# Performance work log

Measured on AMD Instinct MI355X. Metric: run time of the kernel, lower is better.

## Reference

```python
import jax, jax.numpy as jnp
import numpy as np

N = 100000      # nodes
E = 1000000     # edges per branch
C_IN = 128      # in_channels
C_OUT = 64      # out_channels
BN_EPS = 1e-5


def setup_inputs() -> dict:
    key = jax.random.key(0)
    ks = jax.random.split(key, 8)
    inp = {"x": jax.random.normal(ks[0], (N, C_IN), jnp.float32)}
    for i, name in enumerate(["edge_index_p", "edge_index_s", "edge_index_v"]):
        inp[name] = jax.random.randint(ks[1 + i], (2, E), 0, N, dtype=jnp.int32)
    # input BatchNorm1d affine params
    inp["in_gamma"] = jnp.ones((C_IN,), jnp.float32)
    inp["in_beta"] = jnp.zeros((C_IN,), jnp.float32)
    # per-branch GIN MLP params, stacked over the 3 branches (p, s, v)
    inp["W1"] = jax.random.normal(ks[4], (3, C_IN, C_OUT), jnp.float32) * 0.05
    inp["b1"] = jnp.zeros((3, C_OUT), jnp.float32)
    inp["W2"] = jax.random.normal(ks[5], (3, C_OUT, C_OUT), jnp.float32) * 0.05
    inp["b2"] = jnp.zeros((3, C_OUT), jnp.float32)
    # per-branch output BatchNorm1d affine params
    inp["bn_gamma"] = jnp.ones((3, C_OUT), jnp.float32)
    inp["bn_beta"] = jnp.zeros((3, C_OUT), jnp.float32)
    return inp


def _batchnorm(h, gamma, beta):
    # training-mode BatchNorm1d: batch stats over the node dim, biased variance
    mu = h.mean(axis=0)
    var = ((h - mu) ** 2).mean(axis=0)
    return gamma * (h - mu) * jax.lax.rsqrt(var + BN_EPS) + beta


def reference(x, edge_index_p, edge_index_s, edge_index_v,
              in_gamma, in_beta, W1, b1, W2, b2, bn_gamma, bn_beta):
    n = x.shape[0]
    xn = _batchnorm(x, in_gamma, in_beta)  # in_norm
    outs = []
    for i, ei in enumerate([edge_index_p, edge_index_s, edge_index_v]):
        src, dst = ei[0], ei[1]
        # GINConv (eps=0): sum-aggregate neighbor features, add self
        agg = jax.ops.segment_sum(xn[src], dst, num_segments=n)  # [N, C_IN]
        h = xn + agg
        # MLP([C_IN, C_OUT, C_OUT]) with ReLU between, plain last layer
        h = jax.nn.relu(h @ W1[i] + b1[i])
        h = h @ W2[i] + b2[i]
        # post-GIN BatchNorm1d + Tanh
        outs.append(jnp.tanh(_batchnorm(h, bn_gamma[i], bn_beta[i])))
    return tuple(outs)  # (x_p, x_s, x_v)
```

## Files before the change

### kernel.cpp

```cpp
#include <hip/hip_runtime.h>
#include <math.h>

#define NN   100000
#define NE   1000000
#define CIN  128
#define COUT 64
#define BN_EPS 1e-5f
#define NB    391
#define NBLK1 128
#define CHUNK_E ((NE + NBLK1 - 1) / NBLK1)
#define NT    32
#define NTILE (NN / NT)

#define Y1B_OFF    0
#define COL_OFF    9600000
#define ROWPTR_OFF 12600000
#define OFF_OFF    12900016
#define W1P_OFF    13050160
#define C1_OFF     (W1P_OFF + 3*CIN*COUT)
#define INSUM_OFF  (C1_OFF + 3*COUT)
#define INSQ_OFF   (INSUM_OFF + CIN)
#define OSUM_OFF   (INSQ_OFF + CIN)
#define OSQ_OFF    (OSUM_OFF + 3*COUT)
#define SCALE_OFF  (OSQ_OFF + 3*COUT)
#define SHIFT_OFF  (SCALE_OFF + CIN)
#define OBNS_OFF   (SHIFT_OFF + CIN)
#define OBNB_OFF   (OBNS_OFF + 3*COUT)
#define ZERO_OFF   INSUM_OFF
#define ZERO_CNT   (2*CIN + 6*COUT)

__device__ __forceinline__ unsigned bf16_rne(float f) {
    unsigned u = __float_as_uint(f);
    return (u + 0x7FFFu + ((u >> 16) & 1u)) >> 16;
}
__device__ __forceinline__ float lo16f(unsigned u) { return __uint_as_float(u << 16); }
__device__ __forceinline__ float hi16f(unsigned u) { return __uint_as_float(u & 0xFFFF0000u); }

__global__ __launch_bounds__(256) void k_in_stats(const float* __restrict__ x,
                                                  float* __restrict__ ws) {
    int tid = blockIdx.x * blockDim.x + threadIdx.x;
    int c = tid & (CIN - 1);
    int r0 = tid >> 7;
    int rstride = (gridDim.x * blockDim.x) >> 7;
    float s = 0.f, ss = 0.f;
    for (int r = r0; r < NN; r += rstride) {
        float v = x[(size_t)r * CIN + c];
        s += v; ss += v * v;
    }
    unsafeAtomicAdd(&ws[INSUM_OFF + c], s);
    unsafeAtomicAdd(&ws[INSQ_OFF + c], ss);
}

__global__ void k_in_finalize(const float* __restrict__ g, const float* __restrict__ b,
                              float* __restrict__ ws) {
    int c = threadIdx.x;
    float mu  = ws[INSUM_OFF + c] * (1.f / NN);
    float var = ws[INSQ_OFF + c] * (1.f / NN) - mu * mu;
    float sc  = g[c] * rsqrtf(var + BN_EPS);
    ws[SCALE_OFF + c] = sc;
    ws[SHIFT_OFF + c] = b[c] - mu * sc;
}

__global__ void k_fold(const float* __restrict__ W1, float* __restrict__ ws) {
    int idx = blockIdx.x * blockDim.x + threadIdx.x;
    int k = (idx >> 6) & (CIN - 1);
    ws[W1P_OFF + idx] = ws[SCALE_OFF + k] * W1[idx];
}

__global__ void k_c1(const float* __restrict__ W1, float* __restrict__ ws) {
    int i = blockIdx.x, o = threadIdx.x;
    float acc = 0.f;
    for (int k = 0; k < CIN; ++k)
        acc = fmaf(ws[SHIFT_OFF + k], W1[i * CIN * COUT + k * COUT + o], acc);
    ws[C1_OFF + i * COUT + o] = acc;
}

__global__ __launch_bounds__(256) void k_sort_hist(const int* __restrict__ e0,
                                                   const int* __restrict__ e1,
                                                   const int* __restrict__ e2,
                                                   int* __restrict__ wsi) {
    int z = blockIdx.y;
    const int* ei = (z == 0) ? e0 : (z == 1) ? e1 : e2;
    __shared__ int h[NB];
    for (int i = threadIdx.x; i < NB; i += 256) h[i] = 0;
    __syncthreads();
    int beg = blockIdx.x * CHUNK_E;
    int end = min(NE, beg + CHUNK_E);
    for (int e = beg + threadIdx.x; e < end; e += 256)
        atomicAdd(&h[ei[NE + e] >> 8], 1);
    __syncthreads();
    int* off = wsi + OFF_OFF + z * (NB * NBLK1);
    for (int i = threadIdx.x; i < NB; i += 256)
        off[i * NBLK1 + blockIdx.x] = h[i];
}

__global__ __launch_bounds__(1024) void k_sort_scan(int* __restrict__ wsi) {
    int z = blockIdx.x;
    int* off = wsi + OFF_OFF + z * (NB * NBLK1);
    const int TOT = NB * NBLK1;
    const int CH = (TOT + 1023) / 1024;
    __shared__ int sh[1024];
    int t = threadIdx.x;
    int base = t * CH;
    int s = 0;
    for (int i = 0; i < CH; ++i) {
        int idx = base + i;
        if (idx < TOT) s += off[idx];
    }
    sh[t] = s;
    __syncthreads();
    for (int o = 1; o < 1024; o <<= 1) {
        int v = (t >= o) ? sh[t - o] : 0;
        __syncthreads();
        sh[t] += v;
        __syncthreads();
    }
    int run = sh[t] - s;
    for (int i = 0; i < CH; ++i) {
        int idx = base + i;
        if (idx < TOT) {
            int v = off[idx];
            off[idx] = run;
            run += v;
        }
    }
}

__global__ __launch_bounds__(256) void k_sort_scatter(const int* __restrict__ e0,
                                                      const int* __restrict__ e1,
                                                      const int* __restrict__ e2,
                                                      int* __restrict__ wsi) {
    int z = blockIdx.y;
    const int* ei = (z == 0) ? e0 : (z == 1) ? e1 : e2;
    const int* off = wsi + OFF_OFF + z * (NB * NBLK1);
    unsigned* temp = (unsigned*)wsi + (size_t)z * NE;
    __shared__ int cur[NB];
    for (int i = threadIdx.x; i < NB; i += 256)
        cur[i] = off[i * NBLK1 + blockIdx.x];
    __syncthreads();
    int beg = blockIdx.x * CHUNK_E;
    int end = min(NE, beg + CHUNK_E);
    for (int e = beg + threadIdx.x; e < end; e += 256) {
        int d = ei[NE + e];
        int s = ei[e];
        int pos = atomicAdd(&cur[d >> 8], 1);
        temp[pos] = ((unsigned)(d & 255) << 24) | (unsigned)s;
    }
}

__global__ __launch_bounds__(256) void k_bucket(int* __restrict__ wsi) {
    int z = blockIdx.y, bk = blockIdx.x;
    const int* off = wsi + OFF_OFF + z * (NB * NBLK1);
    const unsigned* temp = (const unsigned*)wsi + (size_t)z * NE;
    int* col    = wsi + COL_OFF + z * NE;
    int* rowptr = wsi + ROWPTR_OFF + z * (NN + 1);
    int bs = off[bk * NBLK1];
    int be = (bk + 1 < NB) ? off[(bk + 1) * NBLK1] : NE;
    __shared__ int h[256], sc[256], cur[256];
    int t = threadIdx.x;
    h[t] = 0;
    __syncthreads();
    for (int e = bs + t; e < be; e += 256)
        atomicAdd(&h[temp[e] >> 24], 1);
    __syncthreads();
    int v = h[t];
    sc[t] = v;
    __syncthreads();
    for (int o = 1; o < 256; o <<= 1) {
        int u = (t >= o) ? sc[t - o] : 0;
        __syncthreads();
        sc[t] += u;
        __syncthreads();
    }
    int excl = sc[t] - v;
    int gd = bk * 256 + t;
    if (gd <= NN) rowptr[gd] = bs + excl;
    cur[t] = excl;
    __syncthreads();
    for (int e = bs + t; e < be; e += 256) {
        unsigned p = temp[e];
        int pos = atomicAdd(&cur[p >> 24], 1);
        col[bs + pos] = (int)(p & 0x00FFFFFFu);
    }
}

__global__ __launch_bounds__(256, 2) void k_gemm1(const float* __restrict__ x,
                                                  const float* __restrict__ W1p_all,
                                                  const float* __restrict__ c1_all,
                                                  unsigned* __restrict__ y1b_all) {
    int lane = threadIdx.x & 63;
    int wave = (blockIdx.x * blockDim.x + threadIdx.x) >> 6;
    int nw   = (gridDim.x * blockDim.x) >> 6;
    float c1v0 = c1_all[lane];
    float c1v1 = c1_all[COUT + lane];
    float c1v2 = c1_all[2 * COUT + lane];
    const int NGRP = NN / 8;
    for (int g = wave; g < NGRP; g += nw) {
        int n0 = __builtin_amdgcn_readfirstlane(g) * 8;
        const float* __restrict__ xr = x + (size_t)n0 * CIN;
        float a0[8], a1[8], a2[8];
        #pragma unroll
        for (int i = 0; i < 8; ++i) { a0[i] = c1v0; a1[i] = c1v1; a2[i] = c1v2; }
        #pragma unroll 1
        for (int kc = 0; kc < CIN; kc += 16) {
            float w0[16], w1[16], w2[16];
            #pragma unroll
            for (int j = 0; j < 16; ++j) {
                w0[j] = W1p_all[(kc + j) * COUT + lane];
                w1[j] = W1p_all[CIN * COUT + (kc + j) * COUT + lane];
                w2[j] = W1p_all[2 * CIN * COUT + (kc + j) * COUT + lane];
            }
            #pragma unroll
            for (int i = 0; i < 8; ++i) {
                #pragma unroll
                for (int j = 0; j < 16; ++j) {
                    float xv = xr[i * CIN + kc + j];
                    a0[i] = fmaf(xv, w0[j], a0[i]);
                    a1[i] = fmaf(xv, w1[j], a1[i]);
                    a2[i] = fmaf(xv, w2[j], a2[i]);
                }
            }
        }
        #define STORE_NODE(zz, az, i) { \
            float vhi_ = __shfl(az[i], (lane & 31) + 32); \
            if (lane < 32) { \
                unsigned wrd_ = bf16_rne(az[i]) | (bf16_rne(vhi_) << 16); \
                y1b_all[((size_t)(zz) * NN + n0 + (i)) * 32 + lane] = wrd_; \
            } }
        #pragma unroll
        for (int i = 0; i < 8; ++i) {
            STORE_NODE(0, a0, i)
            STORE_NODE(1, a1, i)
            STORE_NODE(2, a2, i)
        }
        #undef STORE_NODE
    }
}

__global__ __launch_bounds__(256) void k_gather(const float* __restrict__ b1all,
                                                float* __restrict__ tall,
                                                float* __restrict__ ws) {
    int z = blockIdx.y;
    const unsigned* __restrict__ y1b = (const unsigned*)ws + Y1B_OFF + (size_t)z * NN * 32;
    float* __restrict__ t = tall + (size_t)z * NN * COUT;
    const int* __restrict__ rowptr = (const int*)ws + ROWPTR_OFF + z * (NN + 1);
    const int* __restrict__ col    = (const int*)ws + COL_OFF + z * NE;
    int lane = threadIdx.x & 63;
    int w32  = lane & 31;
    int half = lane >> 5;
    float b1lo = b1all[z * COUT + w32];
    float b1hi = b1all[z * COUT + 32 + w32];
    int wave = (blockIdx.x * blockDim.x + threadIdx.x) >> 6;
    int nw   = (gridDim.x * blockDim.x) >> 6;
    const int NP = NN / 2;
    for (int p = wave; p < NP; p += nw) {
        int n = p * 2 + half;
        int beg = rowptr[n], end = rowptr[n + 1];
        unsigned su = y1b[(size_t)n * 32 + w32];
        float alo = lo16f(su), ahi = hi16f(su);
        float blo = 0.f, bhi = 0.f, clo = 0.f, chi = 0.f, dlo = 0.f, dhi = 0.f;
        int j = beg;
        for (; j + 3 < end; j += 4) {
            int c0 = col[j], c1 = col[j + 1], c2 = col[j + 2], c3 = col[j + 3];
            unsigned u0 = y1b[(size_t)c0 * 32 + w32];
            unsigned u1 = y1b[(size_t)c1 * 32 + w32];
            unsigned u2 = y1b[(size_t)c2 * 32 + w32];
            unsigned u3 = y1b[(size_t)c3 * 32 + w32];
            alo += lo16f(u0); ahi += hi16f(u0);
            blo += lo16f(u1); bhi += hi16f(u1);
            clo += lo16f(u2); chi += hi16f(u2);
            dlo += lo16f(u3); dhi += hi16f(u3);
        }
        for (; j < end; ++j) {
            unsigned u = y1b[(size_t)col[j] * 32 + w32];
            alo += lo16f(u); ahi += hi16f(u);
        }
        t[(size_t)n * 64 + w32]      = fmaxf((alo + blo) + (clo + dlo) + b1lo, 0.f);
        t[(size_t)n * 64 + 32 + w32] = fmaxf((ahi + bhi) + (chi + dhi) + b1hi, 0.f);
    }
}

__global__ __launch_bounds__(256) void k_mlp2(const float* __restrict__ W2all,
                                              const float* __restrict__ b2all,
                                              float* __restrict__ outall,
                                              float* __restrict__ ws) {
    int z = blockIdx.y;
    __shared__ float w2s[COUT * COUT];
    __shared__ float ts[NT][COUT];
    const float* __restrict__ W2 = W2all + z * COUT * COUT;
    float* __restrict__ out = outall + (size_t)z * NN * COUT;
    int tid = threadIdx.x;
    for (int i = tid; i < COUT * COUT; i += 256) w2s[i] = W2[i];
    int lane = tid & 63;
    int wave = tid >> 6;
    int n0 = wave * 8;
    float b2v = b2all[z * COUT + lane];
    float ls = 0.f, lss = 0.f;
    float4 r0, r1;
    {
        const float4* __restrict__ src =
            (const float4*)(out + (size_t)blockIdx.x * NT * COUT);
        r0 = src[tid];
        r1 = src[tid + 256];
    }
    for (int tile = blockIdx.x; tile < NTILE; tile += gridDim.x) {
        __syncthreads();
        {
            float4* dst = (float4*)ts;
            dst[tid] = r0;
            dst[tid + 256] = r1;
        }
        __syncthreads();
        int nxt = tile + gridDim.x;
        if (nxt < NTILE) {
            const float4* __restrict__ src =
                (const float4*)(out + (size_t)nxt * NT * COUT);
            r0 = src[tid];
            r1 = src[tid + 256];
        }
        float a0 = b2v, a1 = b2v, a2 = b2v, a3 = b2v;
        float a4 = b2v, a5 = b2v, a6 = b2v, a7 = b2v;
        #pragma unroll
        for (int jq = 0; jq < 16; ++jq) {
            float wj0 = w2s[(4 * jq)     * COUT + lane];
            float wj1 = w2s[(4 * jq + 1) * COUT + lane];
            float wj2 = w2s[(4 * jq + 2) * COUT + lane];
            float wj3 = w2s[(4 * jq + 3) * COUT + lane];
            float4 t0 = *(const float4*)&ts[n0 + 0][4 * jq];
            float4 t1 = *(const float4*)&ts[n0 + 1][4 * jq];
            float4 t2 = *(const float4*)&ts[n0 + 2][4 * jq];
            float4 t3 = *(const float4*)&ts[n0 + 3][4 * jq];
            float4 t4 = *(const float4*)&ts[n0 + 4][4 * jq];
            float4 t5 = *(const float4*)&ts[n0 + 5][4 * jq];
            float4 t6 = *(const float4*)&ts[n0 + 6][4 * jq];
            float4 t7 = *(const float4*)&ts[n0 + 7][4 * jq];
            a0 = fmaf(t0.x, wj0, a0); a0 = fmaf(t0.y, wj1, a0);
            a0 = fmaf(t0.z, wj2, a0); a0 = fmaf(t0.w, wj3, a0);
            a1 = fmaf(t1.x, wj0, a1); a1 = fmaf(t1.y, wj1, a1);
            a1 = fmaf(t1.z, wj2, a1); a1 = fmaf(t1.w, wj3, a1);
            a2 = fmaf(t2.x, wj0, a2); a2 = fmaf(t2.y, wj1, a2);
            a2 = fmaf(t2.z, wj2, a2); a2 = fmaf(t2.w, wj3, a2);
            a3 = fmaf(t3.x, wj0, a3); a3 = fmaf(t3.y, wj1, a3);
            a3 = fmaf(t3.z, wj2, a3); a3 = fmaf(t3.w, wj3, a3);
            a4 = fmaf(t4.x, wj0, a4); a4 = fmaf(t4.y, wj1, a4);
            a4 = fmaf(t4.z, wj2, a4); a4 = fmaf(t4.w, wj3, a4);
            a5 = fmaf(t5.x, wj0, a5); a5 = fmaf(t5.y, wj1, a5);
            a5 = fmaf(t5.z, wj2, a5); a5 = fmaf(t5.w, wj3, a5);
            a6 = fmaf(t6.x, wj0, a6); a6 = fmaf(t6.y, wj1, a6);
            a6 = fmaf(t6.z, wj2, a6); a6 = fmaf(t6.w, wj3, a6);
            a7 = fmaf(t7.x, wj0, a7); a7 = fmaf(t7.y, wj1, a7);
            a7 = fmaf(t7.z, wj2, a7); a7 = fmaf(t7.w, wj3, a7);
        }
        size_t base = (size_t)tile * NT * COUT + (size_t)n0 * COUT;
        out[base + lane] = a0;
        out[base + COUT + lane] = a1;
        out[base + 2 * COUT + lane] = a2;
        out[base + 3 * COUT + lane] = a3;
        out[base + 4 * COUT + lane] = a4;
        out[base + 5 * COUT + lane] = a5;
        out[base + 6 * COUT + lane] = a6;
        out[base + 7 * COUT + lane] = a7;
        ls += ((a0 + a1) + (a2 + a3)) + ((a4 + a5) + (a6 + a7));
        lss += ((a0 * a0 + a1 * a1) + (a2 * a2 + a3 * a3))
             + ((a4 * a4 + a5 * a5) + (a6 * a6 + a7 * a7));
    }
    unsafeAtomicAdd(&ws[OSUM_OFF + z * COUT + lane], ls);
    unsafeAtomicAdd(&ws[OSQ_OFF + z * COUT + lane], lss);
}

__global__ void k_obn_final(const float* __restrict__ g, const float* __restrict__ b,
                            float* __restrict__ ws) {
    int br = blockIdx.x;
    int o = threadIdx.x;
    float mu  = ws[OSUM_OFF + br * COUT + o] * (1.f / NN);
    float var = ws[OSQ_OFF  + br * COUT + o] * (1.f / NN) - mu * mu;
    float sc  = g[br * COUT + o] * rsqrtf(var + BN_EPS);
    ws[OBNS_OFF + br * COUT + o] = sc;
    ws[OBNB_OFF + br * COUT + o] = b[br * COUT + o] - mu * sc;
}

__global__ __launch_bounds__(256) void k_apply(float* __restrict__ outall,
                                               const float* __restrict__ ws) {
    int z = blockIdx.y;
    float* out = outall + (size_t)z * NN * COUT;
    const float* __restrict__ sc = ws + OBNS_OFF + z * COUT;
    const float* __restrict__ sh = ws + OBNB_OFF + z * COUT;
    int idx = blockIdx.x * blockDim.x + threadIdx.x;
    int stride = gridDim.x * blockDim.x;
    const int total = NN * COUT / 4;
    float4* o4 = (float4*)out;
    for (int v = idx; v < total; v += stride) {
        int c = (v & 15) * 4;
        float4 f = o4[v];
        f.x = tanhf(fmaf(f.x, sc[c],     sh[c]));
        f.y = tanhf(fmaf(f.y, sc[c + 1], sh[c + 1]));
        f.z = tanhf(fmaf(f.z, sc[c + 2], sh[c + 2]));
        f.w = tanhf(fmaf(f.w, sc[c + 3], sh[c + 3]));
        o4[v] = f;
    }
}

extern "C" void kernel_launch(void* const* d_in, const int* in_sizes, int n_in,
                              void* d_out, int out_size, void* d_ws, size_t ws_size,
                              hipStream_t stream) {
    const float* x   = (const float*)d_in[0];
    const int*   eip = (const int*)d_in[1];
    const int*   eis = (const int*)d_in[2];
    const int*   eiv = (const int*)d_in[3];
    const float* ig  = (const float*)d_in[4];
    const float* ib  = (const float*)d_in[5];
    const float* W1  = (const float*)d_in[6];
    const float* b1  = (const float*)d_in[7];
    const float* W2  = (const float*)d_in[8];
    const float* b2  = (const float*)d_in[9];
    const float* bng = (const float*)d_in[10];
    const float* bnb = (const float*)d_in[11];
    float* out = (float*)d_out;
    float* ws  = (float*)d_ws;
    int*   wsi = (int*)d_ws;

    hipMemsetAsync(ws + ZERO_OFF, 0, ZERO_CNT * sizeof(float), stream);

    k_in_stats<<<256, 256, 0, stream>>>(x, ws);
    k_in_finalize<<<1, 128, 0, stream>>>(ig, ib, ws);
    k_fold<<<96, 256, 0, stream>>>(W1, ws);
    k_c1<<<3, 64, 0, stream>>>(W1, ws);

    k_sort_hist<<<dim3(NBLK1, 3), 256, 0, stream>>>(eip, eis, eiv, wsi);
    k_sort_scan<<<3, 1024, 0, stream>>>(wsi);
    k_sort_scatter<<<dim3(NBLK1, 3), 256, 0, stream>>>(eip, eis, eiv, wsi);
    k_bucket<<<dim3(NB, 3), 256, 0, stream>>>(wsi);

    k_gemm1<<<1024, 256, 0, stream>>>(x, ws + W1P_OFF, ws + C1_OFF,
                                      (unsigned*)ws + Y1B_OFF);
    k_gather<<<dim3(2048, 3), 256, 0, stream>>>(b1, out, ws);
    k_mlp2<<<dim3(512, 3), 256, 0, stream>>>(W2, b2, out, ws);
    k_obn_final<<<3, 64, 0, stream>>>(bng, bnb, ws);
    k_apply<<<dim3(1024, 3), 256, 0, stream>>>(out, ws);
}
```

Before: 548.4 us.

## Rewrite second GEMM as per-lane row matvec and split out BN stats

The second MLP layer now assigns one node row per lane. Each lane loads its 64-element row into registers and computes outputs in four groups of 16, reading W2 through scalar/uniform loads instead of LDS. This removes the shared-memory staging and barriers. The output BatchNorm sum and sum-of-squares reduction moves into a separate kernel that rereads the full output, which adds an extra pass over 3x100000x64 floats plus a launch. Per-lane strided row loads are uncoalesced and register pressure is high.

```diff
diff --git a/kernel.cpp b/kernel.cpp
--- a/kernel.cpp
+++ b/kernel.cpp
@@ -9,8 +9,6 @@
 #define NB    391
 #define NBLK1 128
 #define CHUNK_E ((NE + NBLK1 - 1) / NBLK1)
-#define NT    32
-#define NTILE (NN / NT)
 
 #define Y1B_OFF    0
 #define COL_OFF    9600000
@@ -282,90 +280,68 @@
 
 __global__ __launch_bounds__(256) void k_mlp2(const float* __restrict__ W2all,
                                               const float* __restrict__ b2all,
-                                              float* __restrict__ outall,
-                                              float* __restrict__ ws) {
-    int z = blockIdx.y;
-    __shared__ float w2s[COUT * COUT];
-    __shared__ float ts[NT][COUT];
+                                              float* __restrict__ outall) {
+    int z = blockIdx.y;
     const float* __restrict__ W2 = W2all + z * COUT * COUT;
+    const float* __restrict__ b2 = b2all + z * COUT;
     float* __restrict__ out = outall + (size_t)z * NN * COUT;
-    int tid = threadIdx.x;
-    for (int i = tid; i < COUT * COUT; i += 256) w2s[i] = W2[i];
-    int lane = tid & 63;
-    int wave = tid >> 6;
-    int n0 = wave * 8;
-    float b2v = b2all[z * COUT + lane];
-    float ls = 0.f, lss = 0.f;
-    float4 r0, r1;
-    {
-        const float4* __restrict__ src =
-            (const float4*)(out + (size_t)blockIdx.x * NT * COUT);
-        r0 = src[tid];
-        r1 = src[tid + 256];
-    }
-    for (int tile = blockIdx.x; tile < NTILE; tile += gridDim.x) {
-        __syncthreads();
-        {
-            float4* dst = (float4*)ts;
-            dst[tid] = r0;
-            dst[tid + 256] = r1;
-        }
-        __syncthreads();
-        int nxt = tile + gridDim.x;
-        if (nxt < NTILE) {
-            const float4* __restrict__ src =
-                (const float4*)(out + (size_t)nxt * NT * COUT);
-            r0 = src[tid];
-            r1 = src[tid + 256];
-        }
-        float a0 = b2v, a1 = b2v, a2 = b2v, a3 = b2v;
-        float a4 = b2v, a5 = b2v, a6 = b2v, a7 = b2v;
-        #pragma unroll
-        for (int jq = 0; jq < 16; ++jq) {
-            float wj0 = w2s[(4 * jq)     * COUT + lane];
-            float wj1 = w2s[(4 * jq + 1) * COUT + lane];
-            float wj2 = w2s[(4 * jq + 2) * COUT + lane];
-            float wj3 = w2s[(4 * jq + 3) * COUT + lane];
-            float4 t0 = *(const float4*)&ts[n0 + 0][4 * jq];
-            float4 t1 = *(const float4*)&ts[n0 + 1][4 * jq];
-            float4 t2 = *(const float4*)&ts[n0 + 2][4 * jq];
-            float4 t3 = *(const float4*)&ts[n0 + 3][4 * jq];
-            float4 t4 = *(const float4*)&ts[n0 + 4][4 * jq];
-            float4 t5 = *(const float4*)&ts[n0 + 5][4 * jq];
-            float4 t6 = *(const float4*)&ts[n0 + 6][4 * jq];
-            float4 t7 = *(const float4*)&ts[n0 + 7][4 * jq];
-            a0 = fmaf(t0.x, wj0, a0); a0 = fmaf(t0.y, wj1, a0);
-            a0 = fmaf(t0.z, wj2, a0); a0 = fmaf(t0.w, wj3, a0);
-            a1 = fmaf(t1.x, wj0, a1); a1 = fmaf(t1.y, wj1, a1);
-            a1 = fmaf(t1.z, wj2, a1); a1 = fmaf(t1.w, wj3, a1);
-            a2 = fmaf(t2.x, wj0, a2); a2 = fmaf(t2.y, wj1, a2);
-            a2 = fmaf(t2.z, wj2, a2); a2 = fmaf(t2.w, wj3, a2);
-            a3 = fmaf(t3.x, wj0, a3); a3 = fmaf(t3.y, wj1, a3);
-            a3 = fmaf(t3.z, wj2, a3); a3 = fmaf(t3.w, wj3, a3);
-            a4 = fmaf(t4.x, wj0, a4); a4 = fmaf(t4.y, wj1, a4);
-            a4 = fmaf(t4.z, wj2, a4); a4 = fmaf(t4.w, wj3, a4);
-            a5 = fmaf(t5.x, wj0, a5); a5 = fmaf(t5.y, wj1, a5);
-            a5 = fmaf(t5.z, wj2, a5); a5 = fmaf(t5.w, wj3, a5);
-            a6 = fmaf(t6.x, wj0, a6); a6 = fmaf(t6.y, wj1, a6);
-            a6 = fmaf(t6.z, wj2, a6); a6 = fmaf(t6.w, wj3, a6);
-            a7 = fmaf(t7.x, wj0, a7); a7 = fmaf(t7.y, wj1, a7);
-            a7 = fmaf(t7.z, wj2, a7); a7 = fmaf(t7.w, wj3, a7);
-        }
-        size_t base = (size_t)tile * NT * COUT + (size_t)n0 * COUT;
-        out[base + lane] = a0;
-        out[base + COUT + lane] = a1;
-        out[base + 2 * COUT + lane] = a2;
-        out[base + 3 * COUT + lane] = a3;
-        out[base + 4 * COUT + lane] = a4;
-        out[base + 5 * COUT + lane] = a5;
-        out[base + 6 * COUT + lane] = a6;
-        out[base + 7 * COUT + lane] = a7;
-        ls += ((a0 + a1) + (a2 + a3)) + ((a4 + a5) + (a6 + a7));
-        lss += ((a0 * a0 + a1 * a1) + (a2 * a2 + a3 * a3))
-             + ((a4 * a4 + a5 * a5) + (a6 * a6 + a7 * a7));
-    }
-    unsafeAtomicAdd(&ws[OSUM_OFF + z * COUT + lane], ls);
-    unsafeAtomicAdd(&ws[OSQ_OFF + z * COUT + lane], lss);
+    int lane = threadIdx.x & 63;
+    int wave = (blockIdx.x * blockDim.x + threadIdx.x) >> 6;
+    int nw   = (gridDim.x * blockDim.x) >> 6;
+    const int NTL = (NN + 63) / 64;
+    for (int tl = wave; tl < NTL; tl += nw) {
+        int n = tl * 64 + lane;
+        int nc = (n < NN) ? n : NN - 1;
+        bool valid = (n < NN);
+        const float4* __restrict__ tr = (const float4*)(out + (size_t)nc * COUT);
+        float4 T0 = tr[0],  T1 = tr[1],  T2 = tr[2],  T3 = tr[3];
+        float4 T4 = tr[4],  T5 = tr[5],  T6 = tr[6],  T7 = tr[7];
+        float4 T8 = tr[8],  T9 = tr[9],  T10 = tr[10], T11 = tr[11];
+        float4 T12 = tr[12], T13 = tr[13], T14 = tr[14], T15 = tr[15];
+        float4* __restrict__ ow = (float4*)(out + (size_t)nc * COUT);
+        #pragma unroll 1
+        for (int p = 0; p < 4; ++p) {
+            const float* __restrict__ w2p = W2 + p * 16;
+            float acc[16];
+            #pragma unroll
+            for (int o = 0; o < 16; ++o) acc[o] = b2[p * 16 + o];
+#define FMA16(tj, jj) { float tjv_ = (tj); \
+            _Pragma("unroll") \
+            for (int o = 0; o < 16; ++o) \
+                acc[o] = fmaf(tjv_, w2p[(jj) * COUT + o], acc[o]); }
+#define DO4(Tv, jb) FMA16(Tv.x, 4*(jb)) FMA16(Tv.y, 4*(jb)+1) \
+                    FMA16(Tv.z, 4*(jb)+2) FMA16(Tv.w, 4*(jb)+3)
+            DO4(T0, 0)  DO4(T1, 1)  DO4(T2, 2)  DO4(T3, 3)
+            DO4(T4, 4)  DO4(T5, 5)  DO4(T6, 6)  DO4(T7, 7)
+            DO4(T8, 8)  DO4(T9, 9)  DO4(T10, 10) DO4(T11, 11)
+            DO4(T12, 12) DO4(T13, 13) DO4(T14, 14) DO4(T15, 15)
+#undef DO4
+#undef FMA16
+            if (valid) {
+                ow[p * 4 + 0] = make_float4(acc[0], acc[1], acc[2], acc[3]);
+                ow[p * 4 + 1] = make_float4(acc[4], acc[5], acc[6], acc[7]);
+                ow[p * 4 + 2] = make_float4(acc[8], acc[9], acc[10], acc[11]);
+                ow[p * 4 + 3] = make_float4(acc[12], acc[13], acc[14], acc[15]);
+            }
+        }
+    }
+}
+
+__global__ __launch_bounds__(256) void k_h2_stats(const float* __restrict__ outall,
+                                                  float* __restrict__ ws) {
+    int z = blockIdx.y;
+    const float* __restrict__ h = outall + (size_t)z * NN * COUT;
+    int tid = blockIdx.x * blockDim.x + threadIdx.x;
+    int o = tid & 63;
+    int r0 = tid >> 6;
+    int rs = (gridDim.x * blockDim.x) >> 6;
+    float s = 0.f, ss = 0.f;
+    for (int r = r0; r < NN; r += rs) {
+        float v = h[(size_t)r * COUT + o];
+        s += v; ss += v * v;
+    }
+    unsafeAtomicAdd(&ws[OSUM_OFF + z * COUT + o], s);
+    unsafeAtomicAdd(&ws[OSQ_OFF + z * COUT + o], ss);
 }
 
 __global__ void k_obn_final(const float* __restrict__ g, const float* __restrict__ b,
@@ -434,7 +410,8 @@
     k_gemm1<<<1024, 256, 0, stream>>>(x, ws + W1P_OFF, ws + C1_OFF,
                                       (unsigned*)ws + Y1B_OFF);
     k_gather<<<dim3(2048, 3), 256, 0, stream>>>(b1, out, ws);
-    k_mlp2<<<dim3(512, 3), 256, 0, stream>>>(W2, b2, out, ws);
+    k_mlp2<<<dim3(391, 3), 256, 0, stream>>>(W2, b2, out);
+    k_h2_stats<<<dim3(256, 3), 256, 0, stream>>>(out, ws);
     k_obn_final<<<3, 64, 0, stream>>>(bng, bnb, ws);
     k_apply<<<dim3(1024, 3), 256, 0, stream>>>(out, ws);
 }
```

Measured after the change: 564.5 us. 2.9% more time.
